# Kernel optimization log

Hardware: AMD Instinct MI355X
Metric: run time of the kernel (lower is better)

The kernel has to match this reference:

```python
import jax, jax.numpy as jnp
import numpy as np

L = 2        # layer_depth
H = 128      # rnn_size (== embedding dim)
V = 50257    # vocab_size
B = 100      # batch_size
T = 50       # seq_length


def setup_inputs() -> dict:
    key = jax.random.key(0)
    ks = jax.random.split(key, 8)
    inp = {
        'input_data': jax.random.randint(ks[0], (B, T), 0, V, dtype=jnp.int32),
        # embedding ~ U(-0.08, 0.08) as in the original
        'embedding': jax.random.uniform(ks[1], (V, H), jnp.float32, -0.08, 0.08),
        # per-layer GRU params; input dim == H for every layer
        'gate_k': jax.random.normal(ks[2], (L, 2 * H, 2 * H), jnp.float32) * 0.05,
        'gate_b': jnp.ones((L, 2 * H), jnp.float32),  # TF GRUCell gate bias init = 1.0
        'cand_k': jax.random.normal(ks[3], (L, 2 * H, H), jnp.float32) * 0.05,
        'cand_b': jnp.zeros((L, H), jnp.float32),
        'softmax_w': jax.random.normal(ks[4], (V, H), jnp.float32) * 0.05,
        'softmax_b': jnp.zeros((V,), jnp.float32),
    }
    return inp


def _gru_scan(x_bth, gate_k, gate_b, cand_k, cand_b):
    # x_bth: [B, T, H] embedded inputs. Stacked L-layer GRU, TF GRUCell math:
    #   r,u = sigmoid([x,h] @ Wg + bg);  c = tanh([x, r*h] @ Wc + bc)
    #   h' = u*h + (1-u)*c
    x_tbh = jnp.swapaxes(x_bth, 0, 1)  # [T, B, H]
    h0 = jnp.zeros((L, x_bth.shape[0], H), x_bth.dtype)

    def step(hs, x_t):
        inp = x_t
        new_hs = []
        for l in range(L):
            h = hs[l]
            g = jax.nn.sigmoid(jnp.concatenate([inp, h], -1) @ gate_k[l] + gate_b[l])
            r, u = g[:, :H], g[:, H:]
            c = jnp.tanh(jnp.concatenate([inp, r * h], -1) @ cand_k[l] + cand_b[l])
            h_new = u * h + (1.0 - u) * c
            new_hs.append(h_new)
            inp = h_new
        return jnp.stack(new_hs), inp

    final_state, out_tbh = jax.lax.scan(step, h0, x_tbh)
    return jnp.swapaxes(out_tbh, 0, 1), final_state  # [B, T, H], [L, B, H]


def reference(input_data, embedding, gate_k, gate_b, cand_k, cand_b, softmax_w, softmax_b):
    x = embedding[input_data]                                   # [B, T, H]
    out, _ = _gru_scan(x, gate_k, gate_b, cand_k, cand_b)       # [B, T, H]
    out = out.reshape(-1, H)                                    # [B*T, H]
    logits = out @ softmax_w.T + softmax_b                      # [B*T, V]
    probs = jax.nn.softmax(logits, axis=-1)
    return logits, probs
```

## Files before the change

### kernel.cpp

```cpp
#include <hip/hip_runtime.h>
#include <hip/hip_bf16.h>
#include <math.h>

#define GL 2
#define GH 128
#define GH2 256
#define GV 50257
#define GB 100
#define GT 50
#define GM 5000
#define NT 393
#define MT 40

typedef __attribute__((ext_vector_type(4))) float f32x4;
typedef __attribute__((ext_vector_type(8))) short bf16x8;

__global__ __launch_bounds__(1024) void gru_kernel(
    const int* __restrict__ tok,
    const float* __restrict__ emb,
    const float* __restrict__ gate_k,
    const float* __restrict__ gate_b,
    const float* __restrict__ cand_k,
    const float* __restrict__ cand_b,
    float* __restrict__ out)
{
    const int b = blockIdx.x;
    const int tid = threadIdx.x;

    __shared__ float xin[GH2];
    __shared__ float hs[2][GH];
    __shared__ float g[GH2];
    __shared__ float gpart[4][GH2];
    __shared__ float cpart[8][GH];

    if (tid < GH) { hs[0][tid] = 0.f; hs[1][tid] = 0.f; }
    __syncthreads();

    for (int t = 0; t < GT; ++t) {
        const int token = tok[b * GT + t];
        if (tid < GH) xin[tid] = emb[(size_t)token * GH + tid];

        for (int l = 0; l < GL; ++l) {
            if (tid >= GH && tid < GH2) xin[tid] = hs[l][tid - GH];
            __syncthreads();

            {
                const int j  = tid & 255;
                const int t4 = tid >> 8;
                const float* gcol = gate_k + (size_t)l * GH2 * GH2 + (size_t)(t4 * 64) * GH2 + j;
                const float* xv = xin + t4 * 64;
                float acc = 0.f;
                #pragma unroll 16
                for (int i = 0; i < 64; ++i) acc += xv[i] * gcol[(size_t)i * GH2];
                gpart[t4][j] = acc;
            }
            __syncthreads();
            if (tid < GH2) {
                float s = gpart[0][tid] + gpart[1][tid] + gpart[2][tid] + gpart[3][tid]
                        + gate_b[l * GH2 + tid];
                g[tid] = 1.f / (1.f + expf(-s));
            }
            __syncthreads();
            if (tid >= GH && tid < GH2) xin[tid] = g[tid - GH] * hs[l][tid - GH];
            __syncthreads();

            {
                const int j  = tid & 127;
                const int t8 = tid >> 7;
                const float* ccol = cand_k + (size_t)l * GH2 * GH + (size_t)(t8 * 32) * GH + j;
                const float* xv = xin + t8 * 32;
                float acc = 0.f;
                #pragma unroll 16
                for (int i = 0; i < 32; ++i) acc += xv[i] * ccol[(size_t)i * GH];
                cpart[t8][j] = acc;
            }
            __syncthreads();
            if (tid < GH) {
                float csum = 0.f;
                #pragma unroll
                for (int p = 0; p < 8; ++p) csum += cpart[p][tid];
                const float c = tanhf(csum + cand_b[l * GH + tid]);
                const float u = g[GH + tid];
                const float hn = u * hs[l][tid] + (1.f - u) * c;
                hs[l][tid] = hn;
                xin[tid] = hn;
                if (l == GL - 1) out[(size_t)(b * GT + t) * GH + tid] = hn;
            }
            __syncthreads();
        }
    }
}

__device__ __forceinline__ unsigned short f2bf(float x) {
    union { float f; unsigned u; } c; c.f = x;
    unsigned r = c.u + 0x7FFFu + ((c.u >> 16) & 1u);
    return (unsigned short)(r >> 16);
}
__device__ __forceinline__ float bf2f(unsigned short b) {
    union { unsigned u; float f; } c; c.u = ((unsigned)b) << 16; return c.f;
}

__global__ __launch_bounds__(256) void prep_kernel(
    const float* __restrict__ src, unsigned short* __restrict__ dst,
    int ntiles, int nrows)
{
    const int idx = blockIdx.x * 256 + threadIdx.x;
    if (idx >= ntiles * 4 * 128) return;
    const int r    = idx & 127;
    const int c    = idx >> 7;
    const int cs   = c & 3;
    const int tile = c >> 2;
    int row = tile * 128 + r; if (row > nrows - 1) row = nrows - 1;
    const float* s = src + (size_t)row * GH + (cs & 1) * 64;
    unsigned short* d = dst + (size_t)c * 8192 + r * 64;
    const bool lo = (cs >= 2);
    const int rx = r & 7;

    #pragma unroll
    for (int gq = 0; gq < 8; ++gq) {
        float x[8];
        *(float4*)(x)     = *(const float4*)(s + gq * 8);
        *(float4*)(x + 4) = *(const float4*)(s + gq * 8 + 4);
        unsigned u[4];
        #pragma unroll
        for (int q = 0; q < 4; ++q) {
            const float a0 = x[q * 2], a1 = x[q * 2 + 1];
            const unsigned short hi0 = f2bf(a0), hi1 = f2bf(a1);
            unsigned short h0, h1;
            if (lo) { h0 = f2bf(a0 - bf2f(hi0)); h1 = f2bf(a1 - bf2f(hi1)); }
            else    { h0 = hi0; h1 = hi1; }
            u[q] = (unsigned)h0 | ((unsigned)h1 << 16);
        }
        *(uint4*)(d + (size_t)((gq ^ rx) * 8)) = *(const uint4*)u;
    }
}

__global__ __launch_bounds__(256) void mfma_logits_kernel(
    const unsigned short* __restrict__ Ap, const unsigned short* __restrict__ Wp,
    const float* __restrict__ bias,
    float* __restrict__ logits, float* __restrict__ pmax, float* __restrict__ psum)
{
    __shared__ unsigned short ldsA[8192];
    __shared__ unsigned short ldsW[8192];
    __shared__ float sM[2][128];
    __shared__ float sS[2][128];

    const int bm  = blockIdx.x;
    const int bt  = blockIdx.y;
    const int tid = threadIdx.x;
    const int wid  = tid >> 6;
    const int lane = tid & 63;
    const int wm = wid >> 1, wn = wid & 1;
    const int l15 = lane & 15, l4 = lane >> 4;

    constexpr int amap[6] = {0, 0, 2, 1, 1, 3};
    constexpr int astg[6] = {1, 0, 1, 1, 0, 1};
    constexpr int wmap[6] = {2, 0, 0, 3, 1, 1};
    constexpr int wstg[6] = {1, 1, 0, 1, 1, 0};

    f32x4 acc[4][4];
    #pragma unroll
    for (int i = 0; i < 4; ++i)
        #pragma unroll
        for (int j = 0; j < 4; ++j) acc[i][j] = (f32x4){0.f, 0.f, 0.f, 0.f};

    #pragma unroll
    for (int s = 0; s < 6; ++s) {
        if (astg[s]) {
            const unsigned short* ga = Ap + (size_t)(bm * 4 + amap[s]) * 8192 + wid * 2048 + lane * 8;
            #pragma unroll
            for (int i = 0; i < 4; ++i)
                __builtin_amdgcn_global_load_lds(
                    (const __attribute__((address_space(1))) void*)(ga + i * 512),
                    (__attribute__((address_space(3))) void*)(&ldsA[wid * 2048 + i * 512]), 16, 0, 0);
        }
        if (wstg[s]) {
            const unsigned short* gw = Wp + (size_t)(bt * 4 + wmap[s]) * 8192 + wid * 2048 + lane * 8;
            #pragma unroll
            for (int i = 0; i < 4; ++i)
                __builtin_amdgcn_global_load_lds(
                    (const __attribute__((address_space(1))) void*)(gw + i * 512),
                    (__attribute__((address_space(3))) void*)(&ldsW[wid * 2048 + i * 512]), 16, 0, 0);
        }
        __syncthreads();

        #pragma unroll
        for (int ks = 0; ks < 2; ++ks) {
            bf16x8 af[4], bf[4];
            #pragma unroll
            for (int mi = 0; mi < 4; ++mi) {
                const int row = wm * 64 + mi * 16 + l15;
                const int off = row * 64 + ((ks * 32 + l4 * 8) ^ ((row & 7) << 3));
                af[mi] = *(const bf16x8*)&ldsA[off];
            }
            #pragma unroll
            for (int nj = 0; nj < 4; ++nj) {
                const int row = wn * 64 + nj * 16 + l15;
                const int off = row * 64 + ((ks * 32 + l4 * 8) ^ ((row & 7) << 3));
                bf[nj] = *(const bf16x8*)&ldsW[off];
            }
            #pragma unroll
            for (int mi = 0; mi < 4; ++mi)
                #pragma unroll
                for (int nj = 0; nj < 4; ++nj)
                    acc[mi][nj] = __builtin_amdgcn_mfma_f32_16x16x32_bf16(
                        bf[nj], af[mi], acc[mi][nj], 0, 0, 0);
        }
        __syncthreads();
    }

    const int n0b = bt * 128 + wn * 64;
    float bj4[4][4];
    #pragma unroll
    for (int nj = 0; nj < 4; ++nj) {
        const int nb = n0b + nj * 16 + l4 * 4;
        if (nb + 3 < GV) {
            const float4 t = *(const float4*)&bias[nb];
            bj4[nj][0] = t.x; bj4[nj][1] = t.y; bj4[nj][2] = t.z; bj4[nj][3] = t.w;
        } else {
            #pragma unroll
            for (int r = 0; r < 4; ++r) bj4[nj][r] = (nb + r < GV) ? bias[nb + r] : 0.f;
        }
    }
    #pragma unroll
    for (int mi = 0; mi < 4; ++mi) {
        const int rowb = wm * 64 + mi * 16 + l15;
        const int m = bm * 128 + rowb;
        float v[4][4];
        float mx = -INFINITY;
        #pragma unroll
        for (int nj = 0; nj < 4; ++nj)
            #pragma unroll
            for (int r = 0; r < 4; ++r) {
                v[nj][r] = acc[mi][nj][r] + bj4[nj][r];
                if (n0b + nj * 16 + l4 * 4 + r < GV) mx = fmaxf(mx, v[nj][r]);
            }
        mx = fmaxf(mx, __shfl_xor(mx, 16));
        mx = fmaxf(mx, __shfl_xor(mx, 32));
        float se = 0.f;
        #pragma unroll
        for (int nj = 0; nj < 4; ++nj)
            #pragma unroll
            for (int r = 0; r < 4; ++r)
                if (n0b + nj * 16 + l4 * 4 + r < GV) se += __expf(v[nj][r] - mx);
        se += __shfl_xor(se, 16);
        se += __shfl_xor(se, 32);
        if (m < GM) {
            float* lrow = logits + (size_t)m * GV;
            #pragma unroll
            for (int nj = 0; nj < 4; ++nj) {
                const int nb = n0b + nj * 16 + l4 * 4;
                if (nb + 3 < GV) {
                    float4 st;
                    st.x = v[nj][0]; st.y = v[nj][1]; st.z = v[nj][2]; st.w = v[nj][3];
                    *(float4*)&lrow[nb] = st;
                } else {
                    #pragma unroll
                    for (int r = 0; r < 4; ++r)
                        if (nb + r < GV) lrow[nb + r] = v[nj][r];
                }
            }
        }
        if (l4 == 0) { sM[wn][rowb] = mx; sS[wn][rowb] = se; }
    }
    __syncthreads();
    if (tid < 128) {
        const int m = bm * 128 + tid;
        if (m < GM) {
            const float m0 = sM[0][tid], m1 = sM[1][tid];
            const float M = fmaxf(m0, m1);
            const float S = sS[0][tid] * __expf(m0 - M) + sS[1][tid] * __expf(m1 - M);
            pmax[(size_t)m * NT + bt] = M;
            psum[(size_t)m * NT + bt] = S;
        }
    }
}

__global__ __launch_bounds__(64) void reduce_kernel(
    const float* __restrict__ pmax, const float* __restrict__ psum,
    float* __restrict__ rowM, float* __restrict__ rowInvS)
{
    const int m = blockIdx.x;
    const int lane = threadIdx.x;
    float M = -INFINITY, S = 0.f;
    for (int t = lane; t < NT; t += 64) {
        const float m2 = pmax[(size_t)m * NT + t];
        const float s2 = psum[(size_t)m * NT + t];
        const float nM = fmaxf(M, m2);
        S = S * expf(M - nM) + s2 * expf(m2 - nM);
        M = nM;
    }
    #pragma unroll
    for (int d = 1; d < 64; d <<= 1) {
        const float m2 = __shfl_xor(M, d);
        const float s2 = __shfl_xor(S, d);
        const float nM = fmaxf(M, m2);
        S = S * expf(M - nM) + s2 * expf(m2 - nM);
        M = nM;
    }
    if (lane == 0) { rowM[m] = M; rowInvS[m] = 1.f / S; }
}

__global__ __launch_bounds__(256) void probs_kernel(
    const float* __restrict__ logits,
    const float* __restrict__ rowM, const float* __restrict__ rowInvS,
    float* __restrict__ probs)
{
    const float4* L4 = reinterpret_cast<const float4*>(logits);
    float4* P4 = reinterpret_cast<float4*>(probs);
    const int n4 = (int)(((long long)GM * GV) / 4);
    const int stride = gridDim.x * blockDim.x;
    for (int i = blockIdx.x * blockDim.x + threadIdx.x; i < n4; i += stride) {
        const float4 v = L4[i];
        const int base = i * 4;
        const int m0 = base / GV;
        const int m3 = (base + 3) / GV;
        float4 o;
        if (m0 == m3) {
            const float M = rowM[m0], Is = rowInvS[m0];
            o.x = __expf(v.x - M) * Is;
            o.y = __expf(v.y - M) * Is;
            o.z = __expf(v.z - M) * Is;
            o.w = __expf(v.w - M) * Is;
        } else {
            const int ma = base / GV, mb = (base + 1) / GV;
            const int mc = (base + 2) / GV, md = (base + 3) / GV;
            o.x = __expf(v.x - rowM[ma]) * rowInvS[ma];
            o.y = __expf(v.y - rowM[mb]) * rowInvS[mb];
            o.z = __expf(v.z - rowM[mc]) * rowInvS[mc];
            o.w = __expf(v.w - rowM[md]) * rowInvS[md];
        }
        P4[i] = o;
    }
}

extern "C" void kernel_launch(void* const* d_in, const int* in_sizes, int n_in,
                              void* d_out, int out_size, void* d_ws, size_t ws_size,
                              hipStream_t stream) {
    const int*   tok    = (const int*)d_in[0];
    const float* emb    = (const float*)d_in[1];
    const float* gate_k = (const float*)d_in[2];
    const float* gate_b = (const float*)d_in[3];
    const float* cand_k = (const float*)d_in[4];
    const float* cand_b = (const float*)d_in[5];
    const float* W      = (const float*)d_in[6];
    const float* bias   = (const float*)d_in[7];

    float* logits = (float*)d_out;
    float* probs  = logits + (size_t)GM * GV;

    float* ws = (float*)d_ws;
    float* gruout = ws;
    unsigned short* Ap = (unsigned short*)(gruout + 640000);
    unsigned short* Wp = Ap + (size_t)MT * 4 * 8192;
    float* pmax    = (float*)(Wp + (size_t)NT * 4 * 8192);
    float* psum    = pmax + (size_t)GM * NT;
    float* rowM    = psum + (size_t)GM * NT;
    float* rowInvS = rowM + GM;

    gru_kernel<<<GB, 1024, 0, stream>>>(tok, emb, gate_k, gate_b, cand_k, cand_b, gruout);

    prep_kernel<<<(MT * 4 * 128 + 255) / 256, 256, 0, stream>>>(gruout, Ap, MT, GM);
    prep_kernel<<<(NT * 4 * 128 + 255) / 256, 256, 0, stream>>>(W, Wp, NT, GV);

    dim3 g2(MT, NT);
    mfma_logits_kernel<<<g2, 256, 0, stream>>>(Ap, Wp, bias, logits, pmax, psum);

    reduce_kernel<<<GM, 64, 0, stream>>>(pmax, psum, rowM, rowInvS);

    probs_kernel<<<4096, 256, 0, stream>>>(logits, rowM, rowInvS, probs);
}
```

Before: 1.356 ms.

## Split GRU into batched input projections and per-layer recurrent scans

Moves the input-dependent halves of the gate and candidate matmuls out of the sequential loop into batched xpart kernels covering all timesteps. Layers now run as separate passes, so each scan step only multiplies the hidden state by the recurrent weights. This roughly halves the serial matvec work per step. The cost is extra kernel launches and extra global traffic for the precomputed projections.

```diff
diff --git a/kernel.cpp b/kernel.cpp
--- a/kernel.cpp
+++ b/kernel.cpp
@@ -15,79 +15,127 @@
 typedef __attribute__((ext_vector_type(4))) float f32x4;
 typedef __attribute__((ext_vector_type(8))) short bf16x8;
 
-__global__ __launch_bounds__(1024) void gru_kernel(
-    const int* __restrict__ tok,
-    const float* __restrict__ emb,
-    const float* __restrict__ gate_k,
-    const float* __restrict__ gate_b,
-    const float* __restrict__ cand_k,
-    const float* __restrict__ cand_b,
-    float* __restrict__ out)
+__global__ __launch_bounds__(256) void gather_kernel(
+    const int* __restrict__ tok, const float* __restrict__ emb,
+    float* __restrict__ xb)
+{
+    const int i = blockIdx.x * 256 + threadIdx.x;
+    if (i < GM * 32) {
+        const int m = i >> 5, k4 = (i & 31) * 4;
+        *(float4*)&xb[(size_t)m * GH + k4] =
+            *(const float4*)&emb[(size_t)tok[m] * GH + k4];
+    }
+}
+
+__global__ __launch_bounds__(256) void xpart_kernel(
+    const float* __restrict__ in,
+    const float* __restrict__ gk,
+    const float* __restrict__ ck,
+    float* __restrict__ gx,
+    float* __restrict__ cx)
+{
+    __shared__ float xs[16][128];
+    __shared__ float cpart[2][16][128];
+    const int m0 = blockIdx.x * 16;
+    const int tid = threadIdx.x;
+    #pragma unroll
+    for (int p = 0; p < 8; ++p) {
+        const int idx = p * 256 + tid;
+        const int r = idx >> 7, kq = idx & 127;
+        int m = m0 + r; if (m > GM - 1) m = GM - 1;
+        xs[r][kq] = in[(size_t)m * GH + kq];
+    }
+    __syncthreads();
+    {
+        float acc[16];
+        #pragma unroll
+        for (int r = 0; r < 16; ++r) acc[r] = 0.f;
+        for (int k = 0; k < GH; ++k) {
+            const float w = gk[k * GH2 + tid];
+            #pragma unroll
+            for (int r = 0; r < 16; ++r) acc[r] += xs[r][k] * w;
+        }
+        #pragma unroll
+        for (int r = 0; r < 16; ++r)
+            if (m0 + r < GM) gx[(size_t)(m0 + r) * GH2 + tid] = acc[r];
+    }
+    {
+        const int j = tid & 127, kh = tid >> 7;
+        float acc[16];
+        #pragma unroll
+        for (int r = 0; r < 16; ++r) acc[r] = 0.f;
+        for (int k = kh * 64; k < kh * 64 + 64; ++k) {
+            const float w = ck[k * GH + j];
+            #pragma unroll
+            for (int r = 0; r < 16; ++r) acc[r] += xs[r][k] * w;
+        }
+        #pragma unroll
+        for (int r = 0; r < 16; ++r) cpart[kh][r][j] = acc[r];
+    }
+    __syncthreads();
+    for (int idx = tid; idx < 16 * 128; idx += 256) {
+        const int r = idx >> 7, j = idx & 127;
+        if (m0 + r < GM) cx[(size_t)(m0 + r) * GH + j] = cpart[0][r][j] + cpart[1][r][j];
+    }
+}
+
+__global__ __launch_bounds__(1024) void scan_kernel(
+    const float* __restrict__ gxp,
+    const float* __restrict__ cxp,
+    const float* __restrict__ gkb,
+    const float* __restrict__ ckb,
+    const float* __restrict__ gb,
+    const float* __restrict__ cb,
+    float* __restrict__ hout)
 {
     const int b = blockIdx.x;
     const int tid = threadIdx.x;
-
-    __shared__ float xin[GH2];
-    __shared__ float hs[2][GH];
+    __shared__ float hs[GH];
+    __shared__ float rh[GH];
     __shared__ float g[GH2];
     __shared__ float gpart[4][GH2];
     __shared__ float cpart[8][GH];
-
-    if (tid < GH) { hs[0][tid] = 0.f; hs[1][tid] = 0.f; }
+    if (tid < GH) hs[tid] = 0.f;
     __syncthreads();
-
     for (int t = 0; t < GT; ++t) {
-        const int token = tok[b * GT + t];
-        if (tid < GH) xin[tid] = emb[(size_t)token * GH + tid];
-
-        for (int l = 0; l < GL; ++l) {
-            if (tid >= GH && tid < GH2) xin[tid] = hs[l][tid - GH];
-            __syncthreads();
-
-            {
-                const int j  = tid & 255;
-                const int t4 = tid >> 8;
-                const float* gcol = gate_k + (size_t)l * GH2 * GH2 + (size_t)(t4 * 64) * GH2 + j;
-                const float* xv = xin + t4 * 64;
-                float acc = 0.f;
-                #pragma unroll 16
-                for (int i = 0; i < 64; ++i) acc += xv[i] * gcol[(size_t)i * GH2];
-                gpart[t4][j] = acc;
-            }
-            __syncthreads();
-            if (tid < GH2) {
-                float s = gpart[0][tid] + gpart[1][tid] + gpart[2][tid] + gpart[3][tid]
-                        + gate_b[l * GH2 + tid];
-                g[tid] = 1.f / (1.f + expf(-s));
-            }
-            __syncthreads();
-            if (tid >= GH && tid < GH2) xin[tid] = g[tid - GH] * hs[l][tid - GH];
-            __syncthreads();
-
-            {
-                const int j  = tid & 127;
-                const int t8 = tid >> 7;
-                const float* ccol = cand_k + (size_t)l * GH2 * GH + (size_t)(t8 * 32) * GH + j;
-                const float* xv = xin + t8 * 32;
-                float acc = 0.f;
-                #pragma unroll 16
-                for (int i = 0; i < 32; ++i) acc += xv[i] * ccol[(size_t)i * GH];
-                cpart[t8][j] = acc;
-            }
-            __syncthreads();
-            if (tid < GH) {
-                float csum = 0.f;
-                #pragma unroll
-                for (int p = 0; p < 8; ++p) csum += cpart[p][tid];
-                const float c = tanhf(csum + cand_b[l * GH + tid]);
-                const float u = g[GH + tid];
-                const float hn = u * hs[l][tid] + (1.f - u) * c;
-                hs[l][tid] = hn;
-                xin[tid] = hn;
-                if (l == GL - 1) out[(size_t)(b * GT + t) * GH + tid] = hn;
-            }
-            __syncthreads();
-        }
+        const int m = b * GT + t;
+        {
+            const int j = tid & 255, t4 = tid >> 8;
+            const float* col = gkb + (size_t)(t4 * 32) * GH2 + j;
+            float acc = 0.f;
+            #pragma unroll 8
+            for (int i = 0; i < 32; ++i) acc += hs[t4 * 32 + i] * col[(size_t)i * GH2];
+            gpart[t4][j] = acc;
+        }
+        __syncthreads();
+        if (tid < GH2) {
+            const float s = gxp[(size_t)m * GH2 + tid] + gpart[0][tid] + gpart[1][tid]
+                          + gpart[2][tid] + gpart[3][tid] + gb[tid];
+            g[tid] = 1.f / (1.f + expf(-s));
+        }
+        __syncthreads();
+        if (tid < GH) rh[tid] = g[tid] * hs[tid];
+        __syncthreads();
+        {
+            const int j = tid & 127, t8 = tid >> 7;
+            const float* col = ckb + (size_t)(t8 * 16) * GH + j;
+            float acc = 0.f;
+            #pragma unroll 8
+            for (int i = 0; i < 16; ++i) acc += rh[t8 * 16 + i] * col[(size_t)i * GH];
+            cpart[t8][j] = acc;
+        }
+        __syncthreads();
+        if (tid < GH) {
+            float cs = cxp[(size_t)m * GH + tid] + cb[tid];
+            #pragma unroll
+            for (int p = 0; p < 8; ++p) cs += cpart[p][tid];
+            const float c = tanhf(cs);
+            const float u = g[GH + tid];
+            const float hn = u * hs[tid] + (1.f - u) * c;
+            hs[tid] = hn;
+            hout[(size_t)m * GH + tid] = hn;
+        }
+        __syncthreads();
     }
 }
 
@@ -358,7 +406,19 @@
     float* rowM    = psum + (size_t)GM * NT;
     float* rowInvS = rowM + GM;
 
-    gru_kernel<<<GB, 1024, 0, stream>>>(tok, emb, gate_k, gate_b, cand_k, cand_b, gruout);
+    float* XBH0 = pmax;
+    float* GX   = pmax + 640000;
+    float* CX   = pmax + 1920000;
+
+    gather_kernel<<<(GM * 32 + 255) / 256, 256, 0, stream>>>(tok, emb, XBH0);
+    xpart_kernel<<<(GM + 15) / 16, 256, 0, stream>>>(XBH0, gate_k, cand_k, GX, CX);
+    scan_kernel<<<GB, 1024, 0, stream>>>(GX, CX,
+        gate_k + 128 * GH2, cand_k + 128 * GH, gate_b, cand_b, XBH0 );
+    xpart_kernel<<<(GM + 15) / 16, 256, 0, stream>>>(XBH0,
+        gate_k + GH2 * GH2, cand_k + GH2 * GH, GX, CX);
+    scan_kernel<<<GB, 1024, 0, stream>>>(GX, CX,
+        gate_k + GH2 * GH2 + 128 * GH2, cand_k + GH2 * GH + 128 * GH,
+        gate_b + GH2, cand_b + GH, gruout);
 
     prep_kernel<<<(MT * 4 * 128 + 255) / 256, 256, 0, stream>>>(gruout, Ap, MT, GM);
     prep_kernel<<<(NT * 4 * 128 + 255) / 256, 256, 0, stream>>>(W, Wp, NT, GV);
```

New measurement: 1.320 ms. 1.03x faster.
